# Kernel tuning notes

Measured on AMD Instinct MI355X. Metric: run time of the kernel, lower is better.

The kernel has to match this reference:

```python
import jax, jax.numpy as jnp
import numpy as np

BLOCK = 32  # GGUF Q8_0 block size: one scale per 32 int8 quants


def setup_inputs() -> dict:
    key = jax.random.key(0)
    k1, k2, k3, k4 = jax.random.split(key, 4)
    B, S, D_IN, D_OUT = 2, 2048, 4096, 16384
    x = jax.random.normal(k1, (B, S, D_IN), dtype=jnp.float32)
    # Stored quantized weights: unsigned byte codes in [0,255]; dequant as (q-128)*scale
    weight_q = jax.random.randint(k2, (D_OUT, D_IN), 0, 255, dtype=jnp.int32)
    # One positive scale per 32-element block along in_features
    scales = jax.random.uniform(k3, (D_OUT, D_IN // BLOCK), dtype=jnp.float32) * 0.02 + 1e-3
    bias = jax.random.normal(k4, (D_OUT,), dtype=jnp.float32)
    return {"x": x, "weight_q": weight_q, "scales": scales, "bias": bias}


def _dequant(weight_q, scales):
    # weight_q: [O, I] int codes, scales: [O, I/BLOCK] -> fp weight [O, I]
    O, I = weight_q.shape
    q = (weight_q.astype(jnp.float32) - 128.0).reshape(O, I // BLOCK, BLOCK)
    return (q * scales[:, :, None]).reshape(O, I)


def reference(x, weight_q, scales, bias):
    # Fused dequant + matmul: y = x @ dequant(W).T + bias
    w = _dequant(weight_q, scales)  # [O, I]
    y = jnp.einsum("bsi,oi->bso", x, w)
    return y + bias
```

## Files before the change

### kernel.cpp

```cpp
#include <hip/hip_runtime.h>
#include <hip/hip_bf16.h>

typedef __attribute__((ext_vector_type(8))) short short8;
typedef __attribute__((ext_vector_type(4))) float f32x4;

#define AS1 __attribute__((address_space(1)))
#define AS3 __attribute__((address_space(3)))

static __device__ __forceinline__ short f2bf(float f) {
    __hip_bfloat16 h = __float2bfloat16(f);
    union { __hip_bfloat16 h; short s; } u;
    u.h = h;
    return u.s;
}


__global__ __launch_bounds__(256) void prepack_w_kernel(const int* __restrict__ wq,
                                                        const float* __restrict__ scales,
                                                        short* __restrict__ Wb,
                                                        long total8) {
    long i = (long)blockIdx.x * 256 + threadIdx.x;
    if (i >= total8) return;
    const int4* p = (const int4*)wq + i * 2;
    int4 q0 = p[0], q1 = p[1];
    float s = scales[(i * 8) >> 5];
    short8 v;
    v[0] = f2bf((float)(q0.x - 128) * s);
    v[1] = f2bf((float)(q0.y - 128) * s);
    v[2] = f2bf((float)(q0.z - 128) * s);
    v[3] = f2bf((float)(q0.w - 128) * s);
    v[4] = f2bf((float)(q1.x - 128) * s);
    v[5] = f2bf((float)(q1.y - 128) * s);
    v[6] = f2bf((float)(q1.z - 128) * s);
    v[7] = f2bf((float)(q1.w - 128) * s);
    ((short8*)Wb)[i] = v;
}

__global__ __launch_bounds__(256) void prepack_x_kernel(const float* __restrict__ x,
                                                        short* __restrict__ Xb,
                                                        long total8) {
    long i = (long)blockIdx.x * 256 + threadIdx.x;
    if (i >= total8) return;
    const float4* p = (const float4*)x + i * 2;
    float4 f0 = p[0], f1 = p[1];
    short8 v;
    v[0] = f2bf(f0.x); v[1] = f2bf(f0.y); v[2] = f2bf(f0.z); v[3] = f2bf(f0.w);
    v[4] = f2bf(f1.x); v[5] = f2bf(f1.y); v[6] = f2bf(f1.z); v[7] = f2bf(f1.w);
    ((short8*)Xb)[i] = v;
}

__global__ __launch_bounds__(512, 2)
void gemm256_kernel(const float* __restrict__ bias,
                    const short* __restrict__ Xb, const short* __restrict__ Wb,
                    float* __restrict__ out, int M, int N, int K) {
    __shared__ alignas(16) short As[4 * 8192];
    __shared__ alignas(16) short Bs[4 * 8192];

    const int nM = M >> 8, nN = N >> 8;
    int bid = blockIdx.x;
    {
        int nwg = nM * nN;
        if ((nwg & 7) == 0) bid = (bid & 7) * (nwg >> 3) + (bid >> 3);
    }
    int pm, pn;
    {
        const int G = 8;
        if ((nN % G) == 0) {
            int per = nM * G;
            int grp = bid / per, in = bid % per;
            pn = grp * G + (in % G);
            pm = in / G;
        } else { pn = bid % nN; pm = bid / nN; }
    }

    const int tid  = threadIdx.x;
    const int lane = tid & 63;
    const int wid  = tid >> 6;
    const int wm   = wid >> 2;
    const int wn   = wid & 3;
    const int q4   = lane >> 4;
    const int l15  = lane & 15;
    const int lx   = lane & 7;

    const long bm = (long)pm << 8, bn = (long)pn << 8;
    const long Kl = K;
    const int  NT = K >> 6;

    const int rA0 = wm * 8192 + l15 * 64;
    const int rA1 = (2 + wm) * 8192 + l15 * 64;
    const int rB0 = (wn >> 1) * 8192 + ((wn & 1) * 64 + l15) * 64;
    const int rB1 = rB0 + 2 * 8192;
    const int sg0 = (q4 ^ lx) * 8;
    const int sg1 = ((4 + q4) ^ lx) * 8;

    const int chnk    = wid * 1024;
    const int srowrel = wid * 16 + (lane >> 3);
    const int scol    = ((lane & 7) ^ (lane >> 3)) * 8;

    const short* aS00 = Xb + (bm + 0   + srowrel + 0) * Kl + scol;
    const short* aS01 = Xb + (bm + 0   + srowrel + 8) * Kl + scol;
    const short* aS10 = Xb + (bm + 128 + srowrel + 0) * Kl + scol;
    const short* aS11 = Xb + (bm + 128 + srowrel + 8) * Kl + scol;
    const short* bS00 = Wb + (bn + 0   + srowrel + 0) * Kl + scol;
    const short* bS01 = Wb + (bn + 0   + srowrel + 8) * Kl + scol;
    const short* bS10 = Wb + (bn + 128 + srowrel + 0) * Kl + scol;
    const short* bS11 = Wb + (bn + 128 + srowrel + 8) * Kl + scol;

#define STGA(H, PARL, OFF) {                                                          \
    __builtin_amdgcn_global_load_lds((const AS1 void*)(aS##H##0 + (OFF)),             \
        (AS3 void*)&As[((PARL) * 2 + (H)) * 8192 + chnk], 16, 0, 0);                  \
    __builtin_amdgcn_global_load_lds((const AS1 void*)(aS##H##1 + (OFF)),             \
        (AS3 void*)&As[((PARL) * 2 + (H)) * 8192 + chnk + 512], 16, 0, 0); }
#define STGB(H, PARL, OFF) {                                                          \
    __builtin_amdgcn_global_load_lds((const AS1 void*)(bS##H##0 + (OFF)),             \
        (AS3 void*)&Bs[((PARL) * 2 + (H)) * 8192 + chnk], 16, 0, 0);                  \
    __builtin_amdgcn_global_load_lds((const AS1 void*)(bS##H##1 + (OFF)),             \
        (AS3 void*)&Bs[((PARL) * 2 + (H)) * 8192 + chnk + 512], 16, 0, 0); }

#define RDA8(RA, SG) {                                                                \
    ak[0] = *(const short8*)&As[(RA) + 0 * 1024 + (SG)];                              \
    ak[1] = *(const short8*)&As[(RA) + 1 * 1024 + (SG)];                              \
    ak[2] = *(const short8*)&As[(RA) + 2 * 1024 + (SG)];                              \
    ak[3] = *(const short8*)&As[(RA) + 3 * 1024 + (SG)];                              \
    ak[4] = *(const short8*)&As[(RA) + 4 * 1024 + (SG)];                              \
    ak[5] = *(const short8*)&As[(RA) + 5 * 1024 + (SG)];                              \
    ak[6] = *(const short8*)&As[(RA) + 6 * 1024 + (SG)];                              \
    ak[7] = *(const short8*)&As[(RA) + 7 * 1024 + (SG)]; }

#define LDB8(RB) { _Pragma("unroll") for (int n = 0; n < 4; ++n) {                    \
    bfr[n][0] = *(const short8*)&Bs[(RB) + n * 1024 + sg0];                           \
    bfr[n][1] = *(const short8*)&Bs[(RB) + n * 1024 + sg1]; } }

#define MFMA32(KK) { __builtin_amdgcn_s_setprio(1);                                   \
    _Pragma("unroll") for (int mi = 0; mi < 8; ++mi)                                  \
        _Pragma("unroll") for (int n = 0; n < 4; ++n)                                 \
            acc[mi][n] = __builtin_amdgcn_mfma_f32_16x16x32_bf16(                     \
                ak[mi], bfr[n][KK], acc[mi][n], 0, 0, 0);                             \
    __builtin_amdgcn_s_setprio(0); }

#define BAR  __builtin_amdgcn_s_barrier()
#define WLGN(n) { asm volatile("s_waitcnt lgkmcnt(" #n ")" ::: "memory");             \
                  __builtin_amdgcn_sched_barrier(0); }
#define VMC(n)  asm volatile("s_waitcnt vmcnt(" #n ")" ::: "memory")

#define TILE2(RA, RB, APAR_N, BPAR_T, OFF_A, OFF_B, DO_A, DO_B, LAST, DRAIN0) {       \
                                                                   \
    LDB8(RB);                                                                         \
    RDA8(RA, sg0);                                                                    \
    if (DO_A) STGA(0, APAR_N, OFF_A);                                                 \
    WLGN(8); BAR; WLGN(0);                                                            \
    MFMA32(0);                                                                        \
    BAR;                                                                              \
                                                                   \
    RDA8(RA, sg1);                                                                    \
    if (DO_A) STGA(1, APAR_N, OFF_A);                                                 \
    if (DO_B) { STGB(0, BPAR_T, OFF_B); STGB(1, BPAR_T, OFF_B); }                     \
    BAR; WLGN(0);                                                                     \
    MFMA32(1);                                                                        \
    if (!(LAST)) {                                                                    \
        if (DRAIN0) { VMC(0); } else { VMC(4); }                                      \
        BAR;                                                                          \
    } }

    f32x4 acc[8][4];
#pragma unroll
    for (int m = 0; m < 8; ++m)
#pragma unroll
        for (int n = 0; n < 4; ++n) acc[m][n] = (f32x4){0.f, 0.f, 0.f, 0.f};

    short8 ak[8], bfr[4][2];

    STGB(0, 0, 0); STGB(1, 0, 0);
    STGA(0, 0, 0); STGA(1, 0, 0);
    STGB(0, 1, 64); STGB(1, 1, 64);
    VMC(4);
    BAR;

    for (int t = 0; t + 3 < NT; t += 2) {
        const long o1 = ((long)t + 1) << 6;
        const long o2 = o1 + 64;
        const long o3 = o2 + 64;
        TILE2(rA0, rB0, 1, 0, o1, o2, true, true, false, false);
        TILE2(rA1, rB1, 0, 1, o2, o3, true, true, false, false);
    }
    {
        const long o1 = ((long)NT - 1) << 6;
        TILE2(rA0, rB0, 1, 0, o1, 0, true, false, false, true);
        TILE2(rA1, rB1, 0, 1, 0, 0, false, false, true, false);
    }

#pragma unroll
    for (int n = 0; n < 4; ++n) {
        long col = bn + wn * 64 + n * 16 + l15;
        float bv = bias[col];
#pragma unroll
        for (int m = 0; m < 8; ++m) {
            long row = bm + wm * 128 + m * 16 + q4 * 4;
#pragma unroll
            for (int r = 0; r < 4; ++r)
                out[(row + r) * (long)N + col] = acc[m][n][r] + bv;
        }
    }
#undef STGA
#undef STGB
#undef RDA8
#undef LDB8
#undef MFMA32
#undef BAR
#undef WLGN
#undef VMC
#undef TILE2
}


template <bool PRE_A, bool PRE_B>
__global__ __launch_bounds__(256, 2)
void gemm_kernel(const float* __restrict__ x, const int* __restrict__ wq,
                 const float* __restrict__ scales, const float* __restrict__ bias,
                 const short* __restrict__ Xb, const short* __restrict__ Wb,
                 float* __restrict__ out, int M, int N, int K) {
    constexpr int BM = 128, BN = 128, BK = 64;
    __shared__ alignas(16) short As[BM * BK];
    __shared__ alignas(16) short Bs[BN * BK];

    const int nM = M / BM, nN = N / BN;
    int bid = blockIdx.x;
    int pm, pn;
    const int G = 8;
    if ((nN % G) == 0) {
        int per = nM * G;
        int grp = bid / per;
        int in  = bid % per;
        pn = grp * G + (in % G);
        pm = in / G;
    } else {
        pn = bid % nN;
        pm = bid / nN;
    }

    const int tid  = threadIdx.x;
    const int lane = tid & 63;
    const int wv   = tid >> 6;
    const int wm   = (wv >> 1) * 64;
    const int wn   = (wv & 1) * 64;
    const int q    = lane >> 4;
    const int l15  = lane & 15;
    const int sxor = lane & 7;

    const long bm = (long)pm * BM, bn = (long)pn * BN;

    f32x4 acc[4][4];
#pragma unroll
    for (int i = 0; i < 4; ++i)
#pragma unroll
        for (int j = 0; j < 4; ++j) acc[i][j] = (f32x4){0.f, 0.f, 0.f, 0.f};

    const int srow = tid >> 3;
    const int scg  = tid & 7;

    const int sg0   = q ^ sxor;
    const int aOff0 = (wm + l15) * 64 + sg0 * 8;
    const int aOff1 = (wm + l15) * 64 + (sg0 ^ 4) * 8;
    const int bOff0 = (wn + l15) * 64 + sg0 * 8;
    const int bOff1 = (wn + l15) * 64 + (sg0 ^ 4) * 8;

    const int prRow  = lane >> 3;
    const int prGsrc = (lane & 7) ^ (lane >> 3);

    for (int k0 = 0; k0 < K; k0 += BK) {
        if constexpr (PRE_A) {
#pragma unroll
            for (int i = 0; i < 4; ++i) {
                int r = wv * 32 + i * 8 + prRow;
                const short* src = Xb + (bm + r) * (long)K + k0 + prGsrc * 8;
                __builtin_amdgcn_global_load_lds((const AS1 void*)src,
                                                 (AS3 void*)&As[(wv * 32 + i * 8) * 64],
                                                 16, 0, 0);
            }
        } else {
#pragma unroll
            for (int i = 0; i < 4; ++i) {
                int r = i * 32 + srow;
                const float4* p = (const float4*)(x + (bm + r) * (long)K + k0 + scg * 8);
                float4 f0 = p[0], f1 = p[1];
                short8 v;
                v[0] = f2bf(f0.x); v[1] = f2bf(f0.y); v[2] = f2bf(f0.z); v[3] = f2bf(f0.w);
                v[4] = f2bf(f1.x); v[5] = f2bf(f1.y); v[6] = f2bf(f1.z); v[7] = f2bf(f1.w);
                int sg = scg ^ (r & 7);
                *(short8*)&As[r * 64 + sg * 8] = v;
            }
        }
        if constexpr (PRE_B) {
#pragma unroll
            for (int i = 0; i < 4; ++i) {
                int r = wv * 32 + i * 8 + prRow;
                const short* src = Wb + (bn + r) * (long)K + k0 + prGsrc * 8;
                __builtin_amdgcn_global_load_lds((const AS1 void*)src,
                                                 (AS3 void*)&Bs[(wv * 32 + i * 8) * 64],
                                                 16, 0, 0);
            }
        } else {
#pragma unroll
            for (int i = 0; i < 4; ++i) {
                int r = i * 32 + srow;
                const int4* p = (const int4*)(wq + (bn + r) * (long)K + k0 + scg * 8);
                int4 q0 = p[0], q1 = p[1];
                float s = scales[(bn + r) * (long)(K >> 5) + ((k0 + scg * 8) >> 5)];
                short8 v;
                v[0] = f2bf((float)(q0.x - 128) * s);
                v[1] = f2bf((float)(q0.y - 128) * s);
                v[2] = f2bf((float)(q0.z - 128) * s);
                v[3] = f2bf((float)(q0.w - 128) * s);
                v[4] = f2bf((float)(q1.x - 128) * s);
                v[5] = f2bf((float)(q1.y - 128) * s);
                v[6] = f2bf((float)(q1.z - 128) * s);
                v[7] = f2bf((float)(q1.w - 128) * s);
                int sg = scg ^ (r & 7);
                *(short8*)&Bs[r * 64 + sg * 8] = v;
            }
        }
        __syncthreads();

#pragma unroll
        for (int kk = 0; kk < 2; ++kk) {
            short8 a[4], b[4];
            const int aBase = kk ? aOff1 : aOff0;
            const int bBase = kk ? bOff1 : bOff0;
#pragma unroll
            for (int mi = 0; mi < 4; ++mi) a[mi] = *(const short8*)&As[aBase + mi * 16 * 64];
#pragma unroll
            for (int nj = 0; nj < 4; ++nj) b[nj] = *(const short8*)&Bs[bBase + nj * 16 * 64];
#pragma unroll
            for (int mi = 0; mi < 4; ++mi)
#pragma unroll
                for (int nj = 0; nj < 4; ++nj)
                    acc[mi][nj] = __builtin_amdgcn_mfma_f32_16x16x32_bf16(
                        a[mi], b[nj], acc[mi][nj], 0, 0, 0);
        }
        __syncthreads();
    }

#pragma unroll
    for (int nj = 0; nj < 4; ++nj) {
        long col = bn + wn + nj * 16 + l15;
        float bv = bias[col];
#pragma unroll
        for (int mi = 0; mi < 4; ++mi) {
            long row = bm + wm + mi * 16 + q * 4;
#pragma unroll
            for (int r2 = 0; r2 < 4; ++r2)
                out[(row + r2) * (long)N + col] = acc[mi][nj][r2] + bv;
        }
    }
}


extern "C" void kernel_launch(void* const* d_in, const int* in_sizes, int n_in,
                              void* d_out, int out_size, void* d_ws, size_t ws_size,
                              hipStream_t stream) {
    const float* x      = (const float*)d_in[0];
    const int*   wq     = (const int*)d_in[1];
    const float* scales = (const float*)d_in[2];
    const float* bias   = (const float*)d_in[3];
    float*       out    = (float*)d_out;

    const long N = (long)in_sizes[3];
    const long K = (long)in_sizes[1] / N;
    const long M = (long)in_sizes[0] / K;

    const size_t needW = (size_t)N * K * sizeof(short);
    const size_t needX = (size_t)M * K * sizeof(short);

    short* Wb = (short*)d_ws;
    short* Xb = Wb + (size_t)N * K;

    const bool preB = (d_ws != nullptr) && ws_size >= needW;
    const bool preA = preB && ws_size >= (needW + needX);

    if (preB) {
        long t8 = N * K / 8;
        prepack_w_kernel<<<dim3((unsigned)((t8 + 255) / 256)), dim3(256), 0, stream>>>(
            wq, scales, Wb, t8);
    }
    if (preA) {
        long t8 = M * K / 8;
        prepack_x_kernel<<<dim3((unsigned)((t8 + 255) / 256)), dim3(256), 0, stream>>>(
            x, Xb, t8);
    }

    const long NTl = K / 64;
    const bool big = preA && (M % 256 == 0) && (N % 256 == 0) && (K % 64 == 0) &&
                     (NTl >= 4) && (NTl % 2 == 0);

    if (big) {
        dim3 grid((unsigned)((M / 256) * (N / 256))), block(512);
        gemm256_kernel<<<grid, block, 0, stream>>>(bias, Xb, Wb, out, (int)M, (int)N, (int)K);
    } else {
        dim3 grid((unsigned)((M / 128) * (N / 128))), block(256);
        if (preA)
            gemm_kernel<true, true><<<grid, block, 0, stream>>>(x, wq, scales, bias, Xb, Wb,
                                                                out, (int)M, (int)N, (int)K);
        else if (preB)
            gemm_kernel<false, true><<<grid, block, 0, stream>>>(x, wq, scales, bias, Xb, Wb,
                                                                 out, (int)M, (int)N, (int)K);
        else
            gemm_kernel<false, false><<<grid, block, 0, stream>>>(x, wq, scales, bias, Xb, Wb,
                                                                  out, (int)M, (int)N, (int)K);
    }
}
```

Baseline: 600.6 us.

## Simplify GEMM main loop to single-stage double buffering with full drain

Replaces the staggered A/B prefetch schedule, where B ran two tiles ahead and A one tile ahead with partial vmcnt waits and mid-tile barriers, with a simpler scheme. Each tile now issues all A and B global-to-LDS loads for the next tile up front, computes, then fully drains vmcnt and barriers once. This cuts barrier count and the complex wait logic. The cost is less latency hiding, because every tile waits for all outstanding loads before continuing.

```diff
diff --git a/kernel.cpp b/kernel.cpp
--- a/kernel.cpp
+++ b/kernel.cpp
@@ -143,24 +143,17 @@
                   __builtin_amdgcn_sched_barrier(0); }
 #define VMC(n)  asm volatile("s_waitcnt vmcnt(" #n ")" ::: "memory")
 
-#define TILE2(RA, RB, APAR_N, BPAR_T, OFF_A, OFF_B, DO_A, DO_B, LAST, DRAIN0) {       \
-                                                                   \
+#define TILE1(RA, RB, PARN, OFFN, DO_S, LAST) {                                       \
+    if (DO_S) { STGA(0, PARN, OFFN); STGA(1, PARN, OFFN);                             \
+                STGB(0, PARN, OFFN); STGB(1, PARN, OFFN); }                           \
     LDB8(RB);                                                                         \
     RDA8(RA, sg0);                                                                    \
-    if (DO_A) STGA(0, APAR_N, OFF_A);                                                 \
-    WLGN(8); BAR; WLGN(0);                                                            \
+    WLGN(0);                                                                          \
     MFMA32(0);                                                                        \
-    BAR;                                                                              \
-                                                                   \
     RDA8(RA, sg1);                                                                    \
-    if (DO_A) STGA(1, APAR_N, OFF_A);                                                 \
-    if (DO_B) { STGB(0, BPAR_T, OFF_B); STGB(1, BPAR_T, OFF_B); }                     \
-    BAR; WLGN(0);                                                                     \
+    WLGN(0);                                                                          \
     MFMA32(1);                                                                        \
-    if (!(LAST)) {                                                                    \
-        if (DRAIN0) { VMC(0); } else { VMC(4); }                                      \
-        BAR;                                                                          \
-    } }
+    if (!(LAST)) { VMC(0); BAR; } }
 
     f32x4 acc[8][4];
 #pragma unroll
@@ -170,23 +163,21 @@
 
     short8 ak[8], bfr[4][2];
 
+    STGA(0, 0, 0); STGA(1, 0, 0);
     STGB(0, 0, 0); STGB(1, 0, 0);
-    STGA(0, 0, 0); STGA(1, 0, 0);
-    STGB(0, 1, 64); STGB(1, 1, 64);
-    VMC(4);
+    VMC(0);
     BAR;
 
-    for (int t = 0; t + 3 < NT; t += 2) {
+    for (int t = 0; t < NT - 2; t += 2) {
         const long o1 = ((long)t + 1) << 6;
         const long o2 = o1 + 64;
-        const long o3 = o2 + 64;
-        TILE2(rA0, rB0, 1, 0, o1, o2, true, true, false, false);
-        TILE2(rA1, rB1, 0, 1, o2, o3, true, true, false, false);
+        TILE1(rA0, rB0, 1, o1, true, false);
+        TILE1(rA1, rB1, 0, o2, true, false);
     }
     {
         const long o1 = ((long)NT - 1) << 6;
-        TILE2(rA0, rB0, 1, 0, o1, 0, true, false, false, true);
-        TILE2(rA1, rB1, 0, 1, 0, 0, false, false, true, false);
+        TILE1(rA0, rB0, 1, o1, true, false);
+        TILE1(rA1, rB1, 0, 0, false, true);
     }
 
 #pragma unroll
@@ -209,7 +200,7 @@
 #undef BAR
 #undef WLGN
 #undef VMC
-#undef TILE2
+#undef TILE1
 }
 
 
```

After: 637.7 us. +6.2%, slower.

## Stagger k-half order across wave groups and drop mid-tile barrier

Applied to the files above, without the earlier changes.

The 256x256 tile kernel now splits its waves into two groups: one processes the k=0 half of each 64-wide k tile first, the other the k=1 half. Each tile now has one barrier instead of two, and all A staging stores are issued before that barrier. The goal is to spread LDS bank and port traffic across wave groups and cut barrier stalls. The risk is LDS races from removing the intermediate barrier, plus a duplicated k-loop that increases code size.

```diff
diff --git a/kernel.cpp b/kernel.cpp
--- a/kernel.cpp
+++ b/kernel.cpp
@@ -81,6 +81,7 @@
     const int q4   = lane >> 4;
     const int l15  = lane & 15;
     const int lx   = lane & 7;
+    const bool gA  = (wid >> 2) == 0;
 
     const long bm = (long)pm << 8, bn = (long)pn << 8;
     const long Kl = K;
@@ -143,23 +144,35 @@
                   __builtin_amdgcn_sched_barrier(0); }
 #define VMC(n)  asm volatile("s_waitcnt vmcnt(" #n ")" ::: "memory")
 
-#define TILE2(RA, RB, APAR_N, BPAR_T, OFF_A, OFF_B, DO_A, DO_B, LAST, DRAIN0) {       \
-                                                                   \
+#define TILE2G(RA, RB, APAR_N, BPAR_T, OFF_A, OFF_B, DO_A, DO_B, LAST, DRAIN0, SGX, KX, SGY, KY) { \
     LDB8(RB);                                                                         \
-    RDA8(RA, sg0);                                                                    \
-    if (DO_A) STGA(0, APAR_N, OFF_A);                                                 \
-    WLGN(8); BAR; WLGN(0);                                                            \
-    MFMA32(0);                                                                        \
+    RDA8(RA, SGX);                                                                    \
+    if (DO_A) { STGA(0, APAR_N, OFF_A); STGA(1, APAR_N, OFF_A); }                     \
+    WLGN(8);                                                                          \
     BAR;                                                                              \
-                                                                   \
-    RDA8(RA, sg1);                                                                    \
-    if (DO_A) STGA(1, APAR_N, OFF_A);                                                 \
     if (DO_B) { STGB(0, BPAR_T, OFF_B); STGB(1, BPAR_T, OFF_B); }                     \
-    BAR; WLGN(0);                                                                     \
-    MFMA32(1);                                                                        \
+    WLGN(0);                                                                          \
+    MFMA32(KX);                                                                       \
+    RDA8(RA, SGY);                                                                    \
+    WLGN(0);                                                                          \
+    MFMA32(KY);                                                                       \
     if (!(LAST)) {                                                                    \
         if (DRAIN0) { VMC(0); } else { VMC(4); }                                      \
         BAR;                                                                          \
+    } }
+
+#define KLOOP(SGX, KX, SGY, KY) {                                                     \
+    for (int t = 0; t + 3 < NT; t += 2) {                                             \
+        const long o1 = ((long)t + 1) << 6;                                           \
+        const long o2 = o1 + 64;                                                      \
+        const long o3 = o2 + 64;                                                      \
+        TILE2G(rA0, rB0, 1, 0, o1, o2, true, true, false, false, SGX, KX, SGY, KY);   \
+        TILE2G(rA1, rB1, 0, 1, o2, o3, true, true, false, false, SGX, KX, SGY, KY);   \
+    }                                                                                 \
+    {                                                                                 \
+        const long o1 = ((long)NT - 1) << 6;                                          \
+        TILE2G(rA0, rB0, 1, 0, o1, 0, true, false, false, true, SGX, KX, SGY, KY);    \
+        TILE2G(rA1, rB1, 0, 1, 0, 0, false, false, true, false, SGX, KX, SGY, KY);    \
     } }
 
     f32x4 acc[8][4];
@@ -176,18 +189,8 @@
     VMC(4);
     BAR;
 
-    for (int t = 0; t + 3 < NT; t += 2) {
-        const long o1 = ((long)t + 1) << 6;
-        const long o2 = o1 + 64;
-        const long o3 = o2 + 64;
-        TILE2(rA0, rB0, 1, 0, o1, o2, true, true, false, false);
-        TILE2(rA1, rB1, 0, 1, o2, o3, true, true, false, false);
-    }
-    {
-        const long o1 = ((long)NT - 1) << 6;
-        TILE2(rA0, rB0, 1, 0, o1, 0, true, false, false, true);
-        TILE2(rA1, rB1, 0, 1, 0, 0, false, false, true, false);
-    }
+    if (gA) { KLOOP(sg0, 0, sg1, 1); }
+    else    { KLOOP(sg1, 1, sg0, 0); }
 
 #pragma unroll
     for (int n = 0; n < 4; ++n) {
@@ -209,7 +212,8 @@
 #undef BAR
 #undef WLGN
 #undef VMC
-#undef TILE2
+#undef TILE2G
+#undef KLOOP
 }
 
 
```

Result: no change. 606.8 us (median of 2 runs) (+1.0%).
